# Kernel tuning notes

Hardware: AMD Instinct MI355X
Metric: run time of the kernel (lower is better)

The kernel has to match this reference:

```python
import jax, jax.numpy as jnp
import numpy as np

B, L, D, V = 512, 128, 512, 100000

def setup_inputs() -> dict:
    key = jax.random.key(0)
    ks = jax.random.split(key, 8)
    return {
        "t1s": jax.random.randint(ks[0], (B,), 0, V),
        "t2s": jax.random.randint(ks[1], (B,), 0, V),
        "t1_contexts": jax.random.randint(ks[2], (B, L), 0, V),
        "t2_contexts": jax.random.randint(ks[3], (B, L), 0, V),
        "embed_table": jax.random.normal(ks[4], (V, D), dtype=jnp.float32),
        "att_mat": jax.random.normal(ks[5], (D, D), dtype=jnp.float32) * (6.0 / (D + D)) ** 0.5,
        "w_pred": jax.random.normal(ks[6], (D, 1), dtype=jnp.float32) * 0.02,
        "b_pred": jnp.zeros((1,), dtype=jnp.float32),
    }

def _frob_normalize(x):
    # torch.norm(mat, p=2) is the Frobenius norm of the whole (L, D) matrix
    n = jnp.sqrt(jnp.sum(x * x, axis=(1, 2), keepdims=True))
    return x / n

def reference(t1s, t2s, t1_contexts, t2_contexts, embed_table, att_mat, w_pred, b_pred):
    # dropout is identity in eval mode; t1s/t2s embeddings are unused in the
    # 'dynamic' branch (dead code in the original forward).
    A = _frob_normalize(embed_table[t1_contexts])  # (B, L, D)
    Bm = _frob_normalize(embed_table[t2_contexts])  # (B, L, D)
    # batched bilinear attention: tanh(A @ att_mat @ B^T)
    S = jnp.tanh(jnp.einsum('bld,de,bme->blm', A, att_mat, Bm))  # (B, L, L)
    rows = jax.nn.softmax(jnp.mean(S, axis=2), axis=1)  # (B, L)
    cols = jax.nn.softmax(jnp.mean(S, axis=1), axis=1)  # (B, L)
    newA = jnp.einsum('bld,bl->bd', A, rows)   # (B, D)
    newB = jnp.einsum('bld,bl->bd', Bm, cols)  # (B, D)
    logits = ((newA * newB) @ w_pred + b_pred).reshape(-1)  # (B,)
    return logits, S
```

## Files before the change

### kernel.cpp

```cpp
#include <hip/hip_runtime.h>
#include <hip/hip_bf16.h>
#include <stdint.h>

#define NB 512
#define NL 128
#define ND 512

typedef __bf16 bf16;
typedef __bf16 bf16x8 __attribute__((ext_vector_type(8)));
typedef float  f32x4  __attribute__((ext_vector_type(4)));

__global__ __launch_bounds__(256) void k_gather(const int* __restrict__ ctx1,
                                                const int* __restrict__ ctx2,
                                                const float* __restrict__ table,
                                                bf16* __restrict__ d1,
                                                bf16* __restrict__ d2,
                                                float* __restrict__ ss,
                                                const float* __restrict__ att,
                                                bf16* __restrict__ attT) {
    const int b = blockIdx.x, side = blockIdx.y, zc = blockIdx.z, t = threadIdx.x;
    if (side == 2) {
        int chunk = b * 8 + zc;
        if (chunk < 1024) {
            int i = chunk * 256 + t;
            int n = i >> 9, k = i & 511;
            attT[i] = (bf16)att[k * 512 + n];
        }
        return;
    }
    const int* __restrict__ ctx = side ? ctx2 : ctx1;
    bf16* __restrict__ dst = side ? d2 : d1;
    const int base = b * NL;
    const int dv = t & 127, lr = t >> 7;
    float acc = 0.f;
    #pragma unroll
    for (int i = 0; i < 8; ++i) {
        int l = zc * 16 + i * 2 + lr;
        int idx = ctx[base + l];
        float4 v = ((const float4*)table)[(size_t)idx * (ND / 4) + dv];
        acc += v.x * v.x + v.y * v.y + v.z * v.z + v.w * v.w;
        union { bf16 h[4]; uint2 u; } pk;
        pk.h[0] = (bf16)v.x; pk.h[1] = (bf16)v.y;
        pk.h[2] = (bf16)v.z; pk.h[3] = (bf16)v.w;
        *((uint2*)(dst + (size_t)(base + l) * ND) + dv) = pk.u;
    }
    for (int o = 32; o; o >>= 1) acc += __shfl_xor(acc, o);
    __shared__ float red[4];
    if ((t & 63) == 0) red[t >> 6] = acc;
    __syncthreads();
    if (t == 0) atomicAdd(&ss[side * NB + b], red[0] + red[1] + red[2] + red[3]);
}

__global__ __launch_bounds__(256) void k_gemm1(const bf16* __restrict__ A,
                                               const bf16* __restrict__ B,
                                               bf16* __restrict__ Tout) {
    const int id  = blockIdx.x;
    const int xcd = id & 7;
    const int grp = id >> 3;
    const int n0  = (grp & 3) * 128;
    const int b   = (grp >> 2) * 8 + xcd;
    const int arow0 = b * NL;

    __shared__ __align__(16) bf16 As[128 * 64];
    __shared__ __align__(16) bf16 Bs[128 * 64];

    const int tid = threadIdx.x;
    const int lane = tid & 63, w = tid >> 6;
    const int lm = lane & 15, quad = lane >> 4;
    const int wm = (w & 1) * 64, wn = (w >> 1) * 64;

    f32x4 acc[4][4] = {};

    for (int k0 = 0; k0 < ND; k0 += 64) {
        #pragma unroll
        for (int i = 0; i < 4; ++i) {
            int s = w * 256 + i * 64 + lane;
            int r = s >> 3;
            int c = (s & 7) ^ (r & 7);
            const bf16* ga = A + (size_t)(arow0 + r) * ND + k0 + c * 8;
            const bf16* gb = B + (size_t)(n0 + r) * ND + k0 + c * 8;
            __builtin_amdgcn_global_load_lds(
                (const __attribute__((address_space(1))) void*)ga,
                (__attribute__((address_space(3))) void*)(As + (size_t)(w * 256 + i * 64) * 8),
                16, 0, 0);
            __builtin_amdgcn_global_load_lds(
                (const __attribute__((address_space(1))) void*)gb,
                (__attribute__((address_space(3))) void*)(Bs + (size_t)(w * 256 + i * 64) * 8),
                16, 0, 0);
        }
        __syncthreads();
        #pragma unroll
        for (int kk = 0; kk < 2; ++kk) {
            bf16x8 af[4], bfm[4];
            const int ca = (kk * 4 + quad) ^ (lm & 7);
            #pragma unroll
            for (int t4 = 0; t4 < 4; ++t4) {
                af[t4]  = *(const bf16x8*)&As[(wm + t4 * 16 + lm) * 64 + ca * 8];
                bfm[t4] = *(const bf16x8*)&Bs[(wn + t4 * 16 + lm) * 64 + ca * 8];
            }
            #pragma unroll
            for (int im = 0; im < 4; ++im)
                #pragma unroll
                for (int jn = 0; jn < 4; ++jn)
                    acc[im][jn] = __builtin_amdgcn_mfma_f32_16x16x32_bf16(
                        af[im], bfm[jn], acc[im][jn], 0, 0, 0);
        }
        __syncthreads();
    }

    #pragma unroll
    for (int im = 0; im < 4; ++im)
    #pragma unroll
    for (int jn = 0; jn < 4; ++jn)
    #pragma unroll
    for (int p = 0; p < 4; ++p) {
        int m = wm + im * 16 + quad * 4 + p;
        int n = wn + jn * 16 + lm;
        Tout[(size_t)(arow0 + m) * ND + n0 + n] = (bf16)acc[im][jn][p];
    }
}

__global__ __launch_bounds__(256) void k_gemm2_final(
        const bf16* __restrict__ Tin, const bf16* __restrict__ B,
        float* __restrict__ Sout,
        const bf16* __restrict__ Ab, const bf16* __restrict__ Bb,
        const float* __restrict__ ss,
        const float* __restrict__ w_pred, const float* __restrict__ b_pred,
        float* __restrict__ logits) {
    const int b = blockIdx.x;
    const int row0 = b * NL;

    __shared__ __align__(16) char smem[32768];
    bf16* As = (bf16*)smem;
    bf16* Bs = (bf16*)(smem + 16384);
    float* pA = (float*)smem;
    float* pB = (float*)(smem + 16384);
    __shared__ float rowb[2][NL], colb[2][NL];
    __shared__ float wrow[NL], wcol[NL];

    const int tid = threadIdx.x;
    const int lane = tid & 63, w = tid >> 6;
    const int lm = lane & 15, quad = lane >> 4;
    const int wm = (w & 1) * 64, wn = (w >> 1) * 64;

    f32x4 acc[4][4] = {};

    for (int k0 = 0; k0 < ND; k0 += 64) {
        #pragma unroll
        for (int i = 0; i < 4; ++i) {
            int s = w * 256 + i * 64 + lane;
            int r = s >> 3;
            int c = (s & 7) ^ (r & 7);
            const bf16* ga = Tin + (size_t)(row0 + r) * ND + k0 + c * 8;
            const bf16* gb = B   + (size_t)(row0 + r) * ND + k0 + c * 8;
            __builtin_amdgcn_global_load_lds(
                (const __attribute__((address_space(1))) void*)ga,
                (__attribute__((address_space(3))) void*)(As + (size_t)(w * 256 + i * 64) * 8),
                16, 0, 0);
            __builtin_amdgcn_global_load_lds(
                (const __attribute__((address_space(1))) void*)gb,
                (__attribute__((address_space(3))) void*)(Bs + (size_t)(w * 256 + i * 64) * 8),
                16, 0, 0);
        }
        __syncthreads();
        #pragma unroll
        for (int kk = 0; kk < 2; ++kk) {
            bf16x8 af[4], bfm[4];
            const int ca = (kk * 4 + quad) ^ (lm & 7);
            #pragma unroll
            for (int t4 = 0; t4 < 4; ++t4) {
                af[t4]  = *(const bf16x8*)&As[(wm + t4 * 16 + lm) * 64 + ca * 8];
                bfm[t4] = *(const bf16x8*)&Bs[(wn + t4 * 16 + lm) * 64 + ca * 8];
            }
            #pragma unroll
            for (int im = 0; im < 4; ++im)
                #pragma unroll
                for (int jn = 0; jn < 4; ++jn)
                    acc[im][jn] = __builtin_amdgcn_mfma_f32_16x16x32_bf16(
                        af[im], bfm[jn], acc[im][jn], 0, 0, 0);
        }
        __syncthreads();
    }

    const float sc = rsqrtf(ss[b] * ss[NB + b]);
    float* __restrict__ Sb = Sout + (size_t)b * NL * NL;
    #pragma unroll
    for (int im = 0; im < 4; ++im)
    #pragma unroll
    for (int jn = 0; jn < 4; ++jn)
    #pragma unroll
    for (int p = 0; p < 4; ++p) {
        float v = tanhf(acc[im][jn][p] * sc);
        acc[im][jn][p] = v;
        int m = wm + im * 16 + quad * 4 + p;
        int n = wn + jn * 16 + lm;
        __builtin_nontemporal_store(v, &Sb[m * NL + n]);
    }
    #pragma unroll
    for (int im = 0; im < 4; ++im)
    #pragma unroll
    for (int p = 0; p < 4; ++p) {
        float r = acc[im][0][p] + acc[im][1][p] + acc[im][2][p] + acc[im][3][p];
        r += __shfl_xor(r, 1); r += __shfl_xor(r, 2);
        r += __shfl_xor(r, 4); r += __shfl_xor(r, 8);
        if (lm == 0) rowb[wn >> 6][wm + im * 16 + quad * 4 + p] = r;
    }
    #pragma unroll
    for (int jn = 0; jn < 4; ++jn) {
        float cv = 0.f;
        #pragma unroll
        for (int im = 0; im < 4; ++im)
            #pragma unroll
            for (int p = 0; p < 4; ++p) cv += acc[im][jn][p];
        cv += __shfl_xor(cv, 16); cv += __shfl_xor(cv, 32);
        if (quad == 0) colb[wm >> 6][wn + jn * 16 + lm] = cv;
    }
    __syncthreads();

    if (tid < 64) {
        float a  = (rowb[0][tid] + rowb[1][tid]) * (1.f / NL);
        float c2 = (rowb[0][tid + 64] + rowb[1][tid + 64]) * (1.f / NL);
        float mx = fmaxf(a, c2);
        for (int o = 32; o; o >>= 1) mx = fmaxf(mx, __shfl_xor(mx, o));
        float e0 = expf(a - mx), e1 = expf(c2 - mx);
        float s = e0 + e1;
        for (int o = 32; o; o >>= 1) s += __shfl_xor(s, o);
        float inv = 1.f / s;
        wrow[tid] = e0 * inv; wrow[tid + 64] = e1 * inv;
    } else if (tid < 128) {
        int q = tid - 64;
        float a  = (colb[0][q] + colb[1][q]) * (1.f / NL);
        float c2 = (colb[0][q + 64] + colb[1][q + 64]) * (1.f / NL);
        float mx = fmaxf(a, c2);
        for (int o = 32; o; o >>= 1) mx = fmaxf(mx, __shfl_xor(mx, o));
        float e0 = expf(a - mx), e1 = expf(c2 - mx);
        float s = e0 + e1;
        for (int o = 32; o; o >>= 1) s += __shfl_xor(s, o);
        float inv = 1.f / s;
        wcol[q] = e0 * inv; wcol[q + 64] = e1 * inv;
    }
    __syncthreads();

    const int c = tid & 63, g = tid >> 6;
    const bf16* __restrict__ Abase = Ab + (size_t)b * NL * ND;
    const bf16* __restrict__ Bbase = Bb + (size_t)b * NL * ND;
    float aacc[8] = {}, bacc[8] = {};
    for (int l = g; l < NL; l += 4) {
        float wr = wrow[l], wc = wcol[l];
        bf16x8 va = *(const bf16x8*)(Abase + (size_t)l * ND + c * 8);
        bf16x8 vb = *(const bf16x8*)(Bbase + (size_t)l * ND + c * 8);
        #pragma unroll
        for (int j = 0; j < 8; ++j) {
            aacc[j] += wr * (float)va[j];
            bacc[j] += wc * (float)vb[j];
        }
    }
    #pragma unroll
    for (int j = 0; j < 8; ++j) {
        pA[g * ND + c * 8 + j] = aacc[j];
        pB[g * ND + c * 8 + j] = bacc[j];
    }
    __syncthreads();

    if (tid < 64) {
        float dot = 0.f;
        #pragma unroll
        for (int j = 0; j < 8; ++j) {
            int d = tid * 8 + j;
            float na = pA[0 * ND + d] + pA[1 * ND + d] + pA[2 * ND + d] + pA[3 * ND + d];
            float nb = pB[0 * ND + d] + pB[1 * ND + d] + pB[2 * ND + d] + pB[3 * ND + d];
            dot += na * nb * w_pred[d];
        }
        for (int o = 32; o; o >>= 1) dot += __shfl_xor(dot, o);
        if (tid == 0)
            logits[b] = dot * rsqrtf(ss[b]) * rsqrtf(ss[NB + b]) + b_pred[0];
    }
}

extern "C" void kernel_launch(void* const* d_in, const int* in_sizes, int n_in,
                              void* d_out, int out_size, void* d_ws, size_t ws_size,
                              hipStream_t stream) {
    const int*   t1c = (const int*)d_in[2];
    const int*   t2c = (const int*)d_in[3];
    const float* emb = (const float*)d_in[4];
    const float* att = (const float*)d_in[5];
    const float* wp  = (const float*)d_in[6];
    const float* bp  = (const float*)d_in[7];

    float* out    = (float*)d_out;
    float* logits = out;
    float* S      = out + NB;

    char* ws = (char*)d_ws;
    bf16*  Ab   = (bf16*)(ws);
    bf16*  Bb   = (bf16*)(ws + 67108864);
    bf16*  Tb   = (bf16*)(ws + 134217728);
    bf16*  attT = (bf16*)(ws + 201326592);
    float* ss   = (float*)(ws + 201850880);

    hipMemsetAsync(ss, 0, 4096, stream);
    k_gather<<<dim3(NB, 3, 8), 256, 0, stream>>>(t1c, t2c, emb, Ab, Bb, ss, att, attT);
    k_gemm1<<<dim3(2048), 256, 0, stream>>>(Ab, attT, Tb);
    k_gemm2_final<<<dim3(NB), 256, 0, stream>>>(Tb, Bb, S, Ab, Bb, ss, wp, bp, logits);
}
```

Measured before the change: 423.2 us.

## Fuse both GEMMs into one kernel keeping the intermediate in LDS

Merges the A·att GEMM and the T·B^T GEMM plus the softmax epilogue into a single 512-thread kernel per batch item. The 128x512 intermediate is kept in a 128KB swizzled LDS buffer instead of a global workspace, removing one launch and a 64MB bf16 write/read round trip. The cost is heavy LDS use (about 144KB), which allows only one block per CU. Parallelism also drops from 2048 blocks to 512 for the first GEMM, and att tiles are reloaded by every block.

```diff
diff --git a/kernel.cpp b/kernel.cpp
--- a/kernel.cpp
+++ b/kernel.cpp
@@ -51,133 +51,120 @@
     if (t == 0) atomicAdd(&ss[side * NB + b], red[0] + red[1] + red[2] + red[3]);
 }
 
-__global__ __launch_bounds__(256) void k_gemm1(const bf16* __restrict__ A,
-                                               const bf16* __restrict__ B,
-                                               bf16* __restrict__ Tout) {
-    const int id  = blockIdx.x;
-    const int xcd = id & 7;
-    const int grp = id >> 3;
-    const int n0  = (grp & 3) * 128;
-    const int b   = (grp >> 2) * 8 + xcd;
-    const int arow0 = b * NL;
-
-    __shared__ __align__(16) bf16 As[128 * 64];
-    __shared__ __align__(16) bf16 Bs[128 * 64];
-
-    const int tid = threadIdx.x;
-    const int lane = tid & 63, w = tid >> 6;
-    const int lm = lane & 15, quad = lane >> 4;
-    const int wm = (w & 1) * 64, wn = (w >> 1) * 64;
-
-    f32x4 acc[4][4] = {};
-
-    for (int k0 = 0; k0 < ND; k0 += 64) {
-        #pragma unroll
-        for (int i = 0; i < 4; ++i) {
-            int s = w * 256 + i * 64 + lane;
-            int r = s >> 3;
-            int c = (s & 7) ^ (r & 7);
-            const bf16* ga = A + (size_t)(arow0 + r) * ND + k0 + c * 8;
-            const bf16* gb = B + (size_t)(n0 + r) * ND + k0 + c * 8;
-            __builtin_amdgcn_global_load_lds(
-                (const __attribute__((address_space(1))) void*)ga,
-                (__attribute__((address_space(3))) void*)(As + (size_t)(w * 256 + i * 64) * 8),
-                16, 0, 0);
-            __builtin_amdgcn_global_load_lds(
-                (const __attribute__((address_space(1))) void*)gb,
-                (__attribute__((address_space(3))) void*)(Bs + (size_t)(w * 256 + i * 64) * 8),
-                16, 0, 0);
-        }
-        __syncthreads();
-        #pragma unroll
-        for (int kk = 0; kk < 2; ++kk) {
-            bf16x8 af[4], bfm[4];
-            const int ca = (kk * 4 + quad) ^ (lm & 7);
-            #pragma unroll
-            for (int t4 = 0; t4 < 4; ++t4) {
-                af[t4]  = *(const bf16x8*)&As[(wm + t4 * 16 + lm) * 64 + ca * 8];
-                bfm[t4] = *(const bf16x8*)&Bs[(wn + t4 * 16 + lm) * 64 + ca * 8];
-            }
-            #pragma unroll
-            for (int im = 0; im < 4; ++im)
-                #pragma unroll
-                for (int jn = 0; jn < 4; ++jn)
-                    acc[im][jn] = __builtin_amdgcn_mfma_f32_16x16x32_bf16(
-                        af[im], bfm[jn], acc[im][jn], 0, 0, 0);
-        }
-        __syncthreads();
-    }
-
-    #pragma unroll
-    for (int im = 0; im < 4; ++im)
-    #pragma unroll
-    for (int jn = 0; jn < 4; ++jn)
-    #pragma unroll
-    for (int p = 0; p < 4; ++p) {
-        int m = wm + im * 16 + quad * 4 + p;
-        int n = wn + jn * 16 + lm;
-        Tout[(size_t)(arow0 + m) * ND + n0 + n] = (bf16)acc[im][jn][p];
-    }
-}
-
-__global__ __launch_bounds__(256) void k_gemm2_final(
-        const bf16* __restrict__ Tin, const bf16* __restrict__ B,
-        float* __restrict__ Sout,
-        const bf16* __restrict__ Ab, const bf16* __restrict__ Bb,
+__global__ __launch_bounds__(512) void k_fused(
+        const bf16* __restrict__ Ab, const bf16* __restrict__ attT,
+        const bf16* __restrict__ Bb, float* __restrict__ Sout,
         const float* __restrict__ ss,
         const float* __restrict__ w_pred, const float* __restrict__ b_pred,
         float* __restrict__ logits) {
     const int b = blockIdx.x;
     const int row0 = b * NL;
-
-    __shared__ __align__(16) char smem[32768];
-    bf16* As = (bf16*)smem;
-    bf16* Bs = (bf16*)(smem + 16384);
-    float* pA = (float*)smem;
-    float* pB = (float*)(smem + 16384);
-    __shared__ float rowb[2][NL], colb[2][NL];
-    __shared__ float wrow[NL], wcol[NL];
-
     const int tid = threadIdx.x;
     const int lane = tid & 63, w = tid >> 6;
     const int lm = lane & 15, quad = lane >> 4;
-    const int wm = (w & 1) * 64, wn = (w >> 1) * 64;
-
-    f32x4 acc[4][4] = {};
+
+    __shared__ __align__(16) char smem[147456];
+    bf16* Tls = (bf16*)smem;
+    bf16* stA = (bf16*)smem;
+    bf16* stT = (bf16*)(smem + 16384);
+    bf16* Bst = (bf16*)(smem + 131072);
+    float* pA = (float*)smem;
+    float* pB = (float*)(smem + 16384);
+    float* rowb = (float*)(smem + 131072);
+    float* colb = (float*)(smem + 131072 + 2048);
+    float* wrow = (float*)(smem + 131072 + 3072);
+    float* wcol = (float*)(smem + 131072 + 3584);
+
+    const int wm1 = (w & 1) * 64;
+    const int wn1 = (w >> 1) * 128;
+    f32x4 acc1[4][8] = {};
 
     for (int k0 = 0; k0 < ND; k0 += 64) {
         #pragma unroll
-        for (int i = 0; i < 4; ++i) {
-            int s = w * 256 + i * 64 + lane;
-            int r = s >> 3;
-            int c = (s & 7) ^ (r & 7);
-            const bf16* ga = Tin + (size_t)(row0 + r) * ND + k0 + c * 8;
-            const bf16* gb = B   + (size_t)(row0 + r) * ND + k0 + c * 8;
+        for (int i = 0; i < 2; ++i) {
+            int s = i * 512 + tid;
+            int r = s >> 3, c = (s & 7) ^ (r & 7);
             __builtin_amdgcn_global_load_lds(
-                (const __attribute__((address_space(1))) void*)ga,
-                (__attribute__((address_space(3))) void*)(As + (size_t)(w * 256 + i * 64) * 8),
+                (const __attribute__((address_space(1))) void*)(Ab + (size_t)(row0 + r) * ND + k0 + c * 8),
+                (__attribute__((address_space(3))) void*)(stA + (size_t)(i * 512 + w * 64) * 8),
                 16, 0, 0);
+        }
+        #pragma unroll
+        for (int i = 0; i < 8; ++i) {
+            int s = i * 512 + tid;
+            int r = s >> 3, c = (s & 7) ^ (r & 7);
             __builtin_amdgcn_global_load_lds(
-                (const __attribute__((address_space(1))) void*)gb,
-                (__attribute__((address_space(3))) void*)(Bs + (size_t)(w * 256 + i * 64) * 8),
+                (const __attribute__((address_space(1))) void*)(attT + (size_t)r * ND + k0 + c * 8),
+                (__attribute__((address_space(3))) void*)(stT + (size_t)(i * 512 + w * 64) * 8),
                 16, 0, 0);
         }
         __syncthreads();
         #pragma unroll
         for (int kk = 0; kk < 2; ++kk) {
-            bf16x8 af[4], bfm[4];
+            bf16x8 af[4], bfm[8];
             const int ca = (kk * 4 + quad) ^ (lm & 7);
             #pragma unroll
-            for (int t4 = 0; t4 < 4; ++t4) {
-                af[t4]  = *(const bf16x8*)&As[(wm + t4 * 16 + lm) * 64 + ca * 8];
-                bfm[t4] = *(const bf16x8*)&Bs[(wn + t4 * 16 + lm) * 64 + ca * 8];
-            }
+            for (int t4 = 0; t4 < 4; ++t4)
+                af[t4] = *(const bf16x8*)&stA[(wm1 + t4 * 16 + lm) * 64 + ca * 8];
+            #pragma unroll
+            for (int t8 = 0; t8 < 8; ++t8)
+                bfm[t8] = *(const bf16x8*)&stT[(wn1 + t8 * 16 + lm) * 64 + ca * 8];
             #pragma unroll
             for (int im = 0; im < 4; ++im)
                 #pragma unroll
-                for (int jn = 0; jn < 4; ++jn)
-                    acc[im][jn] = __builtin_amdgcn_mfma_f32_16x16x32_bf16(
-                        af[im], bfm[jn], acc[im][jn], 0, 0, 0);
+                for (int jn = 0; jn < 8; ++jn)
+                    acc1[im][jn] = __builtin_amdgcn_mfma_f32_16x16x32_bf16(
+                        af[im], bfm[jn], acc1[im][jn], 0, 0, 0);
+        }
+        __syncthreads();
+    }
+
+    #pragma unroll
+    for (int im = 0; im < 4; ++im)
+    #pragma unroll
+    for (int jn = 0; jn < 8; ++jn)
+    #pragma unroll
+    for (int p = 0; p < 4; ++p) {
+        int m = wm1 + im * 16 + quad * 4 + p;
+        int n = wn1 + jn * 16 + lm;
+        int ks = n >> 6, c = n & 63;
+        int pos = (((c >> 3) ^ (m & 7)) << 3) + (c & 7);
+        Tls[ks * 8192 + m * 64 + pos] = (bf16)acc1[im][jn][p];
+    }
+    __syncthreads();
+
+    const int wm2 = (w & 1) * 64;
+    const int wn2 = (w >> 1) * 32;
+    f32x4 acc2[4][2] = {};
+
+    for (int k0 = 0; k0 < ND; k0 += 64) {
+        #pragma unroll
+        for (int i = 0; i < 2; ++i) {
+            int s = i * 512 + tid;
+            int r = s >> 3, c = (s & 7) ^ (r & 7);
+            __builtin_amdgcn_global_load_lds(
+                (const __attribute__((address_space(1))) void*)(Bb + (size_t)(row0 + r) * ND + k0 + c * 8),
+                (__attribute__((address_space(3))) void*)(Bst + (size_t)(i * 512 + w * 64) * 8),
+                16, 0, 0);
+        }
+        __syncthreads();
+        const bf16* Tk = Tls + (k0 >> 6) * 8192;
+        #pragma unroll
+        for (int kk = 0; kk < 2; ++kk) {
+            bf16x8 af[4], bf2[2];
+            const int ca = (kk * 4 + quad) ^ (lm & 7);
+            #pragma unroll
+            for (int t4 = 0; t4 < 4; ++t4)
+                af[t4] = *(const bf16x8*)&Tk[(wm2 + t4 * 16 + lm) * 64 + ca * 8];
+            #pragma unroll
+            for (int t2 = 0; t2 < 2; ++t2)
+                bf2[t2] = *(const bf16x8*)&Bst[(wn2 + t2 * 16 + lm) * 64 + ca * 8];
+            #pragma unroll
+            for (int im = 0; im < 4; ++im)
+                #pragma unroll
+                for (int jn = 0; jn < 2; ++jn)
+                    acc2[im][jn] = __builtin_amdgcn_mfma_f32_16x16x32_bf16(
+                        af[im], bf2[jn], acc2[im][jn], 0, 0, 0);
         }
         __syncthreads();
     }
@@ -187,39 +174,39 @@
     #pragma unroll
     for (int im = 0; im < 4; ++im)
     #pragma unroll
-    for (int jn = 0; jn < 4; ++jn)
+    for (int jn = 0; jn < 2; ++jn)
     #pragma unroll
     for (int p = 0; p < 4; ++p) {
-        float v = tanhf(acc[im][jn][p] * sc);
-        acc[im][jn][p] = v;
-        int m = wm + im * 16 + quad * 4 + p;
-        int n = wn + jn * 16 + lm;
+        float v = tanhf(acc2[im][jn][p] * sc);
+        acc2[im][jn][p] = v;
+        int m = wm2 + im * 16 + quad * 4 + p;
+        int n = wn2 + jn * 16 + lm;
         __builtin_nontemporal_store(v, &Sb[m * NL + n]);
     }
     #pragma unroll
     for (int im = 0; im < 4; ++im)
     #pragma unroll
     for (int p = 0; p < 4; ++p) {
-        float r = acc[im][0][p] + acc[im][1][p] + acc[im][2][p] + acc[im][3][p];
+        float r = acc2[im][0][p] + acc2[im][1][p];
         r += __shfl_xor(r, 1); r += __shfl_xor(r, 2);
         r += __shfl_xor(r, 4); r += __shfl_xor(r, 8);
-        if (lm == 0) rowb[wn >> 6][wm + im * 16 + quad * 4 + p] = r;
-    }
-    #pragma unroll
-    for (int jn = 0; jn < 4; ++jn) {
+        if (lm == 0) rowb[(w >> 1) * NL + wm2 + im * 16 + quad * 4 + p] = r;
+    }
+    #pragma unroll
+    for (int jn = 0; jn < 2; ++jn) {
         float cv = 0.f;
         #pragma unroll
         for (int im = 0; im < 4; ++im)
             #pragma unroll
-            for (int p = 0; p < 4; ++p) cv += acc[im][jn][p];
+            for (int p = 0; p < 4; ++p) cv += acc2[im][jn][p];
         cv += __shfl_xor(cv, 16); cv += __shfl_xor(cv, 32);
-        if (quad == 0) colb[wm >> 6][wn + jn * 16 + lm] = cv;
+        if (quad == 0) colb[(w & 1) * NL + wn2 + jn * 16 + lm] = cv;
     }
     __syncthreads();
 
     if (tid < 64) {
-        float a  = (rowb[0][tid] + rowb[1][tid]) * (1.f / NL);
-        float c2 = (rowb[0][tid + 64] + rowb[1][tid + 64]) * (1.f / NL);
+        float a  = (rowb[0 * NL + tid] + rowb[1 * NL + tid] + rowb[2 * NL + tid] + rowb[3 * NL + tid]) * (1.f / NL);
+        float c2 = (rowb[0 * NL + tid + 64] + rowb[1 * NL + tid + 64] + rowb[2 * NL + tid + 64] + rowb[3 * NL + tid + 64]) * (1.f / NL);
         float mx = fmaxf(a, c2);
         for (int o = 32; o; o >>= 1) mx = fmaxf(mx, __shfl_xor(mx, o));
         float e0 = expf(a - mx), e1 = expf(c2 - mx);
@@ -229,8 +216,8 @@
         wrow[tid] = e0 * inv; wrow[tid + 64] = e1 * inv;
     } else if (tid < 128) {
         int q = tid - 64;
-        float a  = (colb[0][q] + colb[1][q]) * (1.f / NL);
-        float c2 = (colb[0][q + 64] + colb[1][q + 64]) * (1.f / NL);
+        float a  = (colb[0 * NL + q] + colb[1 * NL + q]) * (1.f / NL);
+        float c2 = (colb[0 * NL + q + 64] + colb[1 * NL + q + 64]) * (1.f / NL);
         float mx = fmaxf(a, c2);
         for (int o = 32; o; o >>= 1) mx = fmaxf(mx, __shfl_xor(mx, o));
         float e0 = expf(a - mx), e1 = expf(c2 - mx);
@@ -245,7 +232,7 @@
     const bf16* __restrict__ Abase = Ab + (size_t)b * NL * ND;
     const bf16* __restrict__ Bbase = Bb + (size_t)b * NL * ND;
     float aacc[8] = {}, bacc[8] = {};
-    for (int l = g; l < NL; l += 4) {
+    for (int l = g; l < NL; l += 8) {
         float wr = wrow[l], wc = wcol[l];
         bf16x8 va = *(const bf16x8*)(Abase + (size_t)l * ND + c * 8);
         bf16x8 vb = *(const bf16x8*)(Bbase + (size_t)l * ND + c * 8);
@@ -267,8 +254,12 @@
         #pragma unroll
         for (int j = 0; j < 8; ++j) {
             int d = tid * 8 + j;
-            float na = pA[0 * ND + d] + pA[1 * ND + d] + pA[2 * ND + d] + pA[3 * ND + d];
-            float nb = pB[0 * ND + d] + pB[1 * ND + d] + pB[2 * ND + d] + pB[3 * ND + d];
+            float na = 0.f, nb = 0.f;
+            #pragma unroll
+            for (int g2 = 0; g2 < 8; ++g2) {
+                na += pA[g2 * ND + d];
+                nb += pB[g2 * ND + d];
+            }
             dot += na * nb * w_pred[d];
         }
         for (int o = 32; o; o >>= 1) dot += __shfl_xor(dot, o);
@@ -294,12 +285,10 @@
     char* ws = (char*)d_ws;
     bf16*  Ab   = (bf16*)(ws);
     bf16*  Bb   = (bf16*)(ws + 67108864);
-    bf16*  Tb   = (bf16*)(ws + 134217728);
-    bf16*  attT = (bf16*)(ws + 201326592);
-    float* ss   = (float*)(ws + 201850880);
+    bf16*  attT = (bf16*)(ws + 134217728);
+    float* ss   = (float*)(ws + 134742016);
 
     hipMemsetAsync(ss, 0, 4096, stream);
     k_gather<<<dim3(NB, 3, 8), 256, 0, stream>>>(t1c, t2c, emb, Ab, Bb, ss, att, attT);
-    k_gemm1<<<dim3(2048), 256, 0, stream>>>(Ab, attT, Tb);
-    k_gemm2_final<<<dim3(NB), 256, 0, stream>>>(Tb, Bb, S, Ab, Bb, ss, wp, bp, logits);
+    k_fused<<<dim3(NB), 512, 0, stream>>>(Ab, attT, Bb, S, ss, wp, bp, logits);
 }
```

Result: faster. 411.8 us (-2.7%).
